# Kernel optimization log

Hardware: AMD Instinct MI355X
Metric: run time of the kernel (lower is better)

Reference implementation:

```python
import jax, jax.numpy as jnp
import numpy as np
from jax import lax

N_NODES = 100000
N_EDGES = 200000
N_GRAPHS = 64
F_IN = 5
HID = 768
EMB = 512
N_LAYERS = 16


def setup_inputs() -> dict:
    key = jax.random.key(0)
    ks = jax.random.split(key, 12)
    s = 0.02
    x = jax.random.normal(ks[0], (N_NODES, F_IN), dtype=jnp.float32)
    edge_index = jax.random.randint(ks[1], (2, N_EDGES), 0, N_NODES, dtype=jnp.int32)
    batch = jnp.sort(jax.random.randint(ks[2], (N_NODES,), 0, N_GRAPHS, dtype=jnp.int32))
    Wp = jax.random.normal(ks[3], (F_IN, HID), dtype=jnp.float32) * s
    bp = jnp.zeros((HID,), dtype=jnp.float32)
    W1 = jax.random.normal(ks[4], (N_LAYERS, HID, HID), dtype=jnp.float32) * s
    b1 = jnp.zeros((N_LAYERS, HID), dtype=jnp.float32)
    W2 = jax.random.normal(ks[5], (N_LAYERS, HID, HID), dtype=jnp.float32) * s
    b2 = jnp.zeros((N_LAYERS, HID), dtype=jnp.float32)
    Wf = jax.random.normal(ks[6], (HID, EMB), dtype=jnp.float32) * s
    bf = jnp.zeros((EMB,), dtype=jnp.float32)
    return {"x": x, "edge_index": edge_index, "batch": batch,
            "Wp": Wp, "bp": bp, "W1": W1, "b1": b1, "W2": W2, "b2": b2,
            "Wf": Wf, "bf": bf}


def reference(x, edge_index, batch, Wp, bp, W1, b1, W2, b2, Wf, bf):
    # input projection: [N, F_IN] -> [N, HID]
    h = x @ Wp + bp
    src, dst = edge_index[0], edge_index[1]

    def layer(h, params):
        w1, bb1, w2, bb2 = params
        # GINConv (eps=0): (1+eps)*x_i + sum_{j->i} x_j, messages flow src -> dst
        agg = jax.ops.segment_sum(h[src], dst, num_segments=N_NODES) + h
        z = jax.nn.relu(agg @ w1 + bb1)
        z = jax.nn.relu(z @ w2 + bb2)
        # outer relu in forward (no-op after ReLU MLP, kept for fidelity)
        return jax.nn.relu(z), None

    h, _ = lax.scan(layer, h, (W1, b1, W2, b2))

    # global mean pool over graphs
    sums = jax.ops.segment_sum(h, batch, num_segments=N_GRAPHS)
    counts = jax.ops.segment_sum(jnp.ones((h.shape[0],), dtype=h.dtype), batch, num_segments=N_GRAPHS)
    pooled = sums / jnp.maximum(counts, 1.0)[:, None]

    return pooled @ Wf + bf
```

## Files before the change

kernel.cpp:

```cpp
#include <hip/hip_runtime.h>

#define HID 768
#define EMB 512
#define NG  64
#define FIN 5
#define NL  16
#define CB  384
#define PSEG 16
#define WPSEG 16

typedef _Float16 f16;
typedef f16   f16x4 __attribute__((ext_vector_type(4)));
typedef f16   f16x8 __attribute__((ext_vector_type(8)));
typedef float f32x4 __attribute__((ext_vector_type(4)));

__global__ void count_deg_k(const int* __restrict__ ei, int* __restrict__ deg, int E) {
    int e = blockIdx.x * 256 + threadIdx.x;
    if (e < E) atomicAdd(&deg[ei[E + e]], 1);
}

__global__ void goff_k(const int* __restrict__ batch, int* __restrict__ goff, int n) {
    int g = threadIdx.x;
    if (g > NG) return;
    if (g == NG) { goff[NG] = n; return; }
    int lo = 0, hi = n;
    while (lo < hi) { int mid = (lo + hi) >> 1; if (batch[mid] < g) lo = mid + 1; else hi = mid; }
    goff[g] = lo;
}

__global__ void scan_rowptr_k(const int* __restrict__ deg, int* __restrict__ rp,
                              int* __restrict__ cur, int n) {
    __shared__ int wsum[16];
    __shared__ int carry;
    int t = threadIdx.x, lane = t & 63, w = t >> 6;
    if (t == 0) carry = 0;
    __syncthreads();
    for (int base = 0; base < n; base += 4096) {
        int v[4]; int s = 0;
        #pragma unroll
        for (int q = 0; q < 4; ++q) { int i = base + t * 4 + q; v[q] = (i < n) ? deg[i] : 0; s += v[q]; }
        int tot = s;
        int sc = tot;
        #pragma unroll
        for (int off = 1; off < 64; off <<= 1) { int u = __shfl_up(sc, off); if (lane >= off) sc += u; }
        if (lane == 63) wsum[w] = sc;
        __syncthreads();
        if (t < 16) {
            int xw = wsum[t];
            #pragma unroll
            for (int off = 1; off < 16; off <<= 1) { int u = __shfl_up(xw, off); if (t >= off) xw += u; }
            wsum[t] = xw;
        }
        __syncthreads();
        int woff = (w > 0) ? wsum[w - 1] : 0;
        int excl = carry + woff + sc - tot;
        #pragma unroll
        for (int q = 0; q < 4; ++q) { int i = base + t * 4 + q; if (i < n) { rp[i] = excl; cur[i] = excl; } excl += v[q]; }
        __syncthreads();
        if (t == 0) carry += wsum[15];
        __syncthreads();
    }
    if (t == 0) rp[n] = carry;
}

__global__ void scatter_k(const int* __restrict__ ei, int* __restrict__ cur,
                          int* __restrict__ csr, int E) {
    int e = blockIdx.x * 256 + threadIdx.x;
    if (e < E) { int d = ei[E + e]; int pos = atomicAdd(&cur[d], 1); csr[pos] = ei[e]; }
}

__global__ void sort_csr_k(const int* __restrict__ rp, int* __restrict__ csr, int n) {
    int i = blockIdx.x * 256 + threadIdx.x;
    if (i >= n) return;
    int e0 = rp[i], e1 = rp[i + 1];
    for (int a = e0 + 1; a < e1; ++a) {
        int v = csr[a];
        int b = a - 1;
        while (b >= e0 && csr[b] > v) { csr[b + 1] = csr[b]; --b; }
        csr[b + 1] = v;
    }
}

__global__ void convert_layer_k(const float* __restrict__ Wa, const float* __restrict__ Wb,
                                f16* __restrict__ wt) {
    __shared__ float tile[64][65];
    const float* src = blockIdx.z ? Wb : Wa;
    f16* dst = wt + (size_t)blockIdx.z * HID * HID;
    int k0 = blockIdx.x * 64, n0 = blockIdx.y * 64;
    int t = threadIdx.x;
    #pragma unroll 4
    for (int i = 0; i < 16; ++i) {
        int r = (t >> 6) + i * 4;
        tile[r][t & 63] = src[(size_t)(k0 + r) * HID + n0 + (t & 63)];
    }
    __syncthreads();
    #pragma unroll 4
    for (int i = 0; i < 16; ++i) {
        int r = (t >> 6) + i * 4;
        dst[(size_t)(n0 + r) * HID + k0 + (t & 63)] = (f16)(tile[t & 63][r] * 64.0f);
    }
}

__global__ void make_wp1_part_k(const float* __restrict__ Wp, const float* __restrict__ bp,
                                const float* __restrict__ W1_0, float* __restrict__ part) {
    int nn = blockIdx.x * 256 + threadIdx.x;
    int s = blockIdx.y;
    if (nn >= HID) return;
    float acc[6] = {0, 0, 0, 0, 0, 0};
    int j0 = s * (HID / WPSEG), j1 = j0 + (HID / WPSEG);
    for (int j = j0; j < j1; ++j) {
        float wj = W1_0[(size_t)j * HID + nn];
        #pragma unroll
        for (int k = 0; k < FIN; ++k) acc[k] += Wp[k * HID + j] * wj;
        acc[5] += bp[j] * wj;
    }
    #pragma unroll
    for (int k = 0; k < 6; ++k) part[((size_t)s * 6 + k) * HID + nn] = acc[k];
}

__global__ void make_wp1_red_k(const float* __restrict__ part, float* __restrict__ wp1) {
    int nn = blockIdx.x * 256 + threadIdx.x;
    if (nn >= HID) return;
    #pragma unroll
    for (int k = 0; k < 6; ++k) {
        float a = 0.0f;
        #pragma unroll
        for (int s = 0; s < WPSEG; ++s) a += part[((size_t)s * 6 + k) * HID + nn];
        wp1[k * HID + nn] = a;
    }
}

__device__ __forceinline__ void row_scale(float amax, float& sc, float& rs) {
    int ex = 10;
    if (amax > 0.0f) frexpf(amax, &ex);
    int sh = 10 - ex;
    sh = sh > 120 ? 120 : (sh < -120 ? -120 : sh);
    sc = ldexpf(1.0f, sh);
    rs = ldexpf(1.0f, -sh);
}

__global__ __launch_bounds__(256) void fused_l0_k(
    const float* __restrict__ x, const int* __restrict__ rp, const int* __restrict__ csr,
    const float* __restrict__ wp1, const float* __restrict__ b1_0,
    f16* __restrict__ h00, f16* __restrict__ h01,
    f16* __restrict__ h10, f16* __restrict__ h11,
    float* __restrict__ rs_out, int nreal, int half) {
    __shared__ float w[7 * HID];
    for (int idx = threadIdx.x; idx < 7 * HID; idx += 256)
        w[idx] = (idx < 6 * HID) ? wp1[idx] : b1_0[idx - 6 * HID];
    __syncthreads();
    int node = blockIdx.x * 4 + (threadIdx.x >> 6);
    int lane = threadIdx.x & 63;
    int cblk = lane >> 5, ll = lane & 31;
    f16* base;
    int rloc;
    if (node < half) { base = cblk ? h10 : h00; rloc = node; }
    else             { base = cblk ? h11 : h01; rloc = node - half; }
    f16* orow = base + (size_t)rloc * CB + ll * 12;
    if (node >= nreal) {
        #pragma unroll
        for (int t = 0; t < 12; ++t) orow[t] = (f16)0.0f;
        if (lane == 0) rs_out[node] = 1.0f;
        return;
    }
    int e0 = rp[node], e1 = rp[node + 1];
    float xa[FIN];
    #pragma unroll
    for (int k = 0; k < FIN; ++k) xa[k] = x[(size_t)node * FIN + k];
    for (int e = e0; e < e1; ++e) {
        int j = csr[e];
        #pragma unroll
        for (int k = 0; k < FIN; ++k) xa[k] += x[(size_t)j * FIN + k];
    }
    float dp1 = (float)(e1 - e0 + 1);
    float a[12];
    #pragma unroll
    for (int t = 0; t < 12; ++t) {
        int c = lane * 12 + t;
        float v = w[5 * HID + c] * dp1 + w[6 * HID + c];
        #pragma unroll
        for (int k = 0; k < FIN; ++k) v += xa[k] * w[k * HID + c];
        a[t] = fmaxf(v, 0.0f);
    }
    float amax = 0.0f;
    #pragma unroll
    for (int t = 0; t < 12; ++t) amax = fmaxf(amax, fabsf(a[t]));
    #pragma unroll
    for (int off = 32; off; off >>= 1) amax = fmaxf(amax, __shfl_xor(amax, off));
    float sc, rs;
    row_scale(amax, sc, rs);
    if (lane == 0) rs_out[node] = rs;
    #pragma unroll
    for (int t = 0; t < 12; ++t) orow[t] = (f16)(a[t] * sc);
}

__global__ __launch_bounds__(256) void aggcol_k(
    const f16* __restrict__ s0, const f16* __restrict__ s1,
    f16* __restrict__ d0, f16* __restrict__ d1,
    const float* __restrict__ rsIn, float inShift,
    float* __restrict__ rsOut, const float* __restrict__ amaxR,
    const int* __restrict__ rp, const int* __restrict__ csr, int nreal, int half,
    int computeScale) {
    int node = blockIdx.x * 8 + (threadIdx.x >> 5);
    int l = threadIdx.x & 31;
    f16* orow = (node < half ? d0 + (size_t)node * CB : d1 + (size_t)(node - half) * CB) + l * 12;
    if (node >= nreal) {
        #pragma unroll
        for (int t = 0; t < 12; ++t) orow[t] = (f16)0.0f;
        if (computeScale && l == 0) rsOut[node] = 1.0f;
        return;
    }
    int e0 = rp[node], e1 = rp[node + 1];
    float invOut;
    if (computeScale) {
        float M = amaxR[node];
        for (int e = e0; e < e1; ++e) M = fmaxf(M, amaxR[csr[e]]);
        float r = 1.0f;
        if (M > 0.0f) {
            int ex; frexpf(M, &ex);
            int sh = ex - 9;
            sh = sh > 120 ? 120 : (sh < -120 ? -120 : sh);
            r = ldexpf(1.0f, sh);
        }
        if (l == 0) rsOut[node] = r;
        invOut = 1.0f / r;
    } else {
        invOut = 1.0f / rsOut[node];
    }
    float a[12];
    {
        float f = rsIn[node] * inShift * invOut;
        const f16* srow = (node < half ? s0 + (size_t)node * CB : s1 + (size_t)(node - half) * CB);
        const f16x4* p = (const f16x4*)(srow + l * 12);
        f16x4 v0 = p[0], v1 = p[1], v2 = p[2];
        #pragma unroll
        for (int t = 0; t < 4; ++t) {
            a[t] = (float)v0[t] * f; a[4 + t] = (float)v1[t] * f; a[8 + t] = (float)v2[t] * f;
        }
    }
    for (int e = e0; e < e1; ++e) {
        int j = csr[e];
        float f = rsIn[j] * inShift * invOut;
        const f16* srow = (j < half ? s0 + (size_t)j * CB : s1 + (size_t)(j - half) * CB);
        const f16x4* p = (const f16x4*)(srow + l * 12);
        f16x4 v0 = p[0], v1 = p[1], v2 = p[2];
        #pragma unroll
        for (int t = 0; t < 4; ++t) {
            a[t] += (float)v0[t] * f; a[4 + t] += (float)v1[t] * f; a[8 + t] += (float)v2[t] * f;
        }
    }
    f16x4 o0, o1, o2;
    #pragma unroll
    for (int t = 0; t < 4; ++t) {
        o0[t] = (f16)a[t]; o1[t] = (f16)a[4 + t]; o2[t] = (f16)a[8 + t];
    }
    f16x4* op = (f16x4*)orow;
    op[0] = o0; op[1] = o1; op[2] = o2;
}

__global__ __launch_bounds__(256) void gemm_seg_k(
    const f16* __restrict__ a0, const f16* __restrict__ a1,
    f16* __restrict__ c0, f16* __restrict__ c1,
    const float* __restrict__ rs, int rsOff, float shiftIn,
    const f16* __restrict__ wt, const float* __restrict__ bias,
    float* __restrict__ amaxR, int recAmax) {
    __shared__ f16 lds[40960];
    const int tid = threadIdx.x;
    const int lane = tid & 63;
    const int wid = tid >> 6;

    const int nwg = gridDim.x;
    const int q = nwg >> 3, r = nwg & 7;
    const int xcd = blockIdx.x & 7, loc = blockIdx.x >> 3;
    const int id2 = (xcd < r ? xcd * (q + 1) : r * (q + 1) + (xcd - r) * q) + loc;
    const int m0 = (id2 / 6) * 128;
    const int n0 = (id2 % 6) * 128;

    const int wr = (wid >> 1) * 64;
    const int wc = (wid & 1) * 64;
    const int lrow = lane >> 3;
    const int usrc = (lane & 7) ^ lrow;
    const int l15 = lane & 15, l4 = lane >> 4;

    auto stageA = [&](int kt, int buf) {
        const f16* abase = (kt < 6) ? a0 : a1;
        const int kb = (kt < 6 ? kt : kt - 6) * 64;
        f16* As = lds + buf * 8192;
        #pragma unroll
        for (int i = 0; i < 4; ++i) {
            int chunk = i * 4 + wid;
            int row = chunk * 8 + lrow;
            const f16* ga = abase + (size_t)(m0 + row) * CB + kb + usrc * 8;
            __builtin_amdgcn_global_load_lds(
                (const __attribute__((address_space(1))) void*)ga,
                (__attribute__((address_space(3))) void*)(As + chunk * 512), 16, 0, 0);
        }
    };
    auto stageB = [&](int kt, int buf) {
        const int kw = kt * 64;
        f16* Bs = lds + 24576 + buf * 8192;
        #pragma unroll
        for (int i = 0; i < 4; ++i) {
            int chunk = i * 4 + wid;
            int row = chunk * 8 + lrow;
            const f16* gb = wt + (size_t)(n0 + row) * HID + kw + usrc * 8;
            __builtin_amdgcn_global_load_lds(
                (const __attribute__((address_space(1))) void*)gb,
                (__attribute__((address_space(3))) void*)(Bs + chunk * 512), 16, 0, 0);
        }
    };

    f32x4 acc[4][4];
    #pragma unroll
    for (int m = 0; m < 4; ++m)
        #pragma unroll
        for (int n = 0; n < 4; ++n) acc[m][n] = (f32x4){0.f, 0.f, 0.f, 0.f};

    stageA(0, 0);
    stageB(0, 0);
    stageA(1, 1);

    #pragma unroll
    for (int t = 0; t < 12; ++t) {
        const f16* Ac = lds + (t % 3) * 8192;
        const f16* Bc = lds + 24576 + (t & 1) * 8192;
        if (t < 11) asm volatile("s_waitcnt vmcnt(4)" ::: "memory");
        else        asm volatile("s_waitcnt vmcnt(0)" ::: "memory");
        __builtin_amdgcn_s_barrier();
        __builtin_amdgcn_sched_barrier(0);
        if (t < 11) stageB(t + 1, (t + 1) & 1);
        if (t < 10) stageA(t + 2, (t + 2) % 3);
        f16x8 af[4][2], bfr[4][2];
        #pragma unroll
        for (int m = 0; m < 4; ++m) {
            int rowH = wr + m * 16 + l15;
            int sw = rowH & 7;
            #pragma unroll
            for (int kk = 0; kk < 2; ++kk) {
                int u = kk * 4 + l4;
                af[m][kk] = *(const f16x8*)(Ac + rowH * 64 + ((u ^ sw) << 3));
            }
        }
        #pragma unroll
        for (int n = 0; n < 4; ++n) {
            int rowB = wc + n * 16 + l15;
            int sw = rowB & 7;
            #pragma unroll
            for (int kk = 0; kk < 2; ++kk) {
                int u = kk * 4 + l4;
                bfr[n][kk] = *(const f16x8*)(Bc + rowB * 64 + ((u ^ sw) << 3));
            }
        }
        __builtin_amdgcn_s_setprio(1);
        #pragma unroll
        for (int kk = 0; kk < 2; ++kk)
            #pragma unroll
            for (int m = 0; m < 4; ++m)
                #pragma unroll
                for (int n = 0; n < 4; ++n)
                    acc[m][n] = __builtin_amdgcn_mfma_f32_16x16x32_f16(af[m][kk], bfr[n][kk], acc[m][n], 0, 0, 0);
        __builtin_amdgcn_s_setprio(0);
    }
    __syncthreads();

    float rvv[16], rinvv[16];
    #pragma unroll
    for (int m = 0; m < 4; ++m)
        #pragma unroll
        for (int r2 = 0; r2 < 4; ++r2) {
            int rowB = wr + m * 16 + (l4 << 2) + r2;
            float rv = rs[rsOff + m0 + rowB] * shiftIn * 8.0f;
            rvv[m * 4 + r2] = rv;
            rinvv[m * 4 + r2] = 1.0f / rv;
        }
    f16* cst = lds;
    float am[16];
    #pragma unroll
    for (int i = 0; i < 16; ++i) am[i] = 0.0f;
    #pragma unroll
    for (int n = 0; n < 4; ++n) {
        const int colB = wc + n * 16 + l15;
        const float bcol = bias[n0 + colB];
        #pragma unroll
        for (int m = 0; m < 4; ++m) {
            #pragma unroll
            for (int r2 = 0; r2 < 4; ++r2) {
                const int rowB = wr + m * 16 + (l4 << 2) + r2;
                float v = acc[m][n][r2] * (1.0f / 512.0f) + bcol * rinvv[m * 4 + r2];
                v = fmaxf(v, 0.0f);
                am[m * 4 + r2] = fmaxf(am[m * 4 + r2], v);
                cst[rowB * 136 + colB] = (f16)v;
            }
        }
    }
    __syncthreads();
    {
        f16* Cw; int csub;
        if (n0 < CB) { Cw = c0; csub = n0; } else { Cw = c1; csub = n0 - CB; }
        #pragma unroll
        for (int i = 0; i < 8; ++i) {
            int rowB = wid * 32 + i * 4 + l4;
            f16x8 vv = *(const f16x8*)&cst[rowB * 136 + l15 * 8];
            *(f16x8*)&Cw[(size_t)(m0 + rowB) * CB + csub + l15 * 8] = vv;
        }
    }
    if (recAmax) {
        #pragma unroll
        for (int i = 0; i < 16; ++i) {
            float a = am[i];
            a = fmaxf(a, __shfl_xor(a, 1));
            a = fmaxf(a, __shfl_xor(a, 2));
            a = fmaxf(a, __shfl_xor(a, 4));
            a = fmaxf(a, __shfl_xor(a, 8));
            if (l15 == 0) {
                int rowB = wr + (i >> 2) * 16 + (l4 << 2) + (i & 3);
                atomicMax((unsigned int*)&amaxR[rsOff + m0 + rowB],
                          __float_as_uint(a * rvv[i]));
            }
        }
    }
}

__global__ __launch_bounds__(256) void pool1_k(
    const f16* __restrict__ h00, const f16* __restrict__ h01,
    const f16* __restrict__ h10, const f16* __restrict__ h11,
    const float* __restrict__ rs,
    const int* __restrict__ goff, float* __restrict__ partial, int half) {
    int g = blockIdx.x, c = blockIdx.y, s = blockIdx.z;
    int t = threadIdx.x;
    int col = c * 256 + t;
    int cb = col >= CB;
    int cc = cb ? col - CB : col;
    int i0 = goff[g], i1 = goff[g + 1];
    int len = i1 - i0;
    int s0 = i0 + (int)(((long long)len * s) / PSEG);
    int s1 = i0 + (int)(((long long)len * (s + 1)) / PSEG);
    float a = 0.0f;
    for (int i = s0; i < s1; ++i) {
        const f16* base = (i < half) ? (cb ? h10 : h00) : (cb ? h11 : h01);
        int r = (i < half) ? i : i - half;
        a += (float)base[(size_t)r * CB + cc] * rs[i];
    }
    partial[((size_t)(g * PSEG + s)) * HID + col] = a;
}

__global__ __launch_bounds__(256) void pool2_k(const float* __restrict__ partial,
                                               float shift, float* __restrict__ pooled) {
    int g = blockIdx.x;
    int col = blockIdx.y * 256 + threadIdx.x;
    float a = 0.0f;
    #pragma unroll
    for (int s = 0; s < PSEG; ++s)
        a += partial[((size_t)(g * PSEG + s)) * HID + col];
    pooled[g * HID + col] = a * shift;
}

__global__ __launch_bounds__(512) void final_mm_k(const float* __restrict__ pooled,
                                                  const int* __restrict__ goff,
                                                  const float* __restrict__ Wf,
                                                  const float* __restrict__ bf,
                                                  float* __restrict__ out) {
    __shared__ float ps[HID];
    int g = blockIdx.x;
    int t = threadIdx.x;
    float inv = 1.0f / fmaxf((float)(goff[g + 1] - goff[g]), 1.0f);
    for (int k = t; k < HID; k += 512) ps[k] = pooled[g * HID + k] * inv;
    __syncthreads();
    float acc = bf[t];
    for (int k = 0; k < HID; ++k) acc += ps[k] * Wf[(size_t)k * EMB + t];
    out[(size_t)g * EMB + t] = acc;
}

__global__ void sentinel_k(float* __restrict__ out, int n, float v) {
    int i = blockIdx.x * 256 + threadIdx.x;
    if (i < n) out[i] = v;
}

extern "C" void kernel_launch(void* const* d_in, const int* in_sizes, int n_in,
                              void* d_out, int out_size, void* d_ws, size_t ws_size,
                              hipStream_t stream) {
    const float* x    = (const float*)d_in[0];
    const int*   ei   = (const int*)d_in[1];
    const int*   batch= (const int*)d_in[2];
    const float* Wp   = (const float*)d_in[3];
    const float* bp   = (const float*)d_in[4];
    const float* W1   = (const float*)d_in[5];
    const float* b1   = (const float*)d_in[6];
    const float* W2   = (const float*)d_in[7];
    const float* b2   = (const float*)d_in[8];
    const float* Wf   = (const float*)d_in[9];
    const float* bf   = (const float*)d_in[10];
    float* out = (float*)d_out;

    const int nreal = in_sizes[0] / FIN;
    const int E     = in_sizes[1] / 2;
    const int npad  = ((nreal + 511) / 512) * 512;
    const int half  = npad / 2;
    const size_t slotsz = (size_t)half * CB;

    char* p = (char*)d_ws;
    auto alloc = [&](size_t bytes) -> char* {
        char* r = p; p += (bytes + 511) & ~(size_t)511; return r;
    };
    f16* slot[6];
    for (int i = 0; i < 6; ++i) slot[i] = (f16*)alloc(slotsz * sizeof(f16));
    f16*   wt   = (f16*)  alloc((size_t)2 * HID * HID * sizeof(f16));
    float* rsA  = (float*)alloc((size_t)npad * sizeof(float));
    float* rsB  = (float*)alloc((size_t)npad * sizeof(float));
    float* amaxR= (float*)alloc((size_t)npad * sizeof(float));
    int*   rp   = (int*)  alloc((size_t)(npad + 1) * sizeof(int));
    int*   csr  = (int*)  alloc((size_t)E * sizeof(int));
    float* wp1  = (float*)alloc((size_t)6 * HID * sizeof(float));
    float* wp1p = (float*)alloc((size_t)WPSEG * 6 * HID * sizeof(float));
    int*   goff = (int*)  alloc((size_t)(NG + 1) * sizeof(int));
    float* pooled = (float*)alloc((size_t)NG * HID * sizeof(float));
    float* partial = (float*)alloc((size_t)NG * PSEG * HID * sizeof(float));
    char*  zstart = p;
    int*   deg  = (int*)  alloc((size_t)npad * sizeof(int));
    int*   cur  = (int*)  alloc((size_t)npad * sizeof(int));
    size_t zbytes = (size_t)(p - zstart);
    size_t need  = (size_t)(p - (char*)d_ws);

    if (need > ws_size) {
        sentinel_k<<<(out_size + 255) / 256, 256, 0, stream>>>(out, out_size, (float)(ws_size >> 20));
        return;
    }

    hipMemsetAsync(zstart, 0, zbytes, stream);

    count_deg_k  <<<(E + 255) / 256, 256, 0, stream>>>(ei, deg, E);
    goff_k       <<<1, 128, 0, stream>>>(batch, goff, nreal);
    scan_rowptr_k<<<1, 1024, 0, stream>>>(deg, rp, cur, nreal);
    scatter_k    <<<(E + 255) / 256, 256, 0, stream>>>(ei, cur, csr, E);
    sort_csr_k   <<<(nreal + 255) / 256, 256, 0, stream>>>(rp, csr, nreal);

    make_wp1_part_k<<<dim3(3, WPSEG), 256, 0, stream>>>(Wp, bp, W1, wp1p);
    make_wp1_red_k <<<3, 256, 0, stream>>>(wp1p, wp1);

    f16 *h00 = slot[0], *h01 = slot[1], *h10 = slot[2], *h11 = slot[3];
    f16 *f0 = slot[4], *f1 = slot[5];

    fused_l0_k<<<npad / 4, 256, 0, stream>>>(x, rp, csr, wp1, b1, h00, h01, h10, h11, rsA, nreal, half);

    const int nwg = (half / 128) * (HID / 128);

    convert_layer_k<<<dim3(HID / 64, HID / 64, 2), 256, 0, stream>>>(W1, W2, wt);
    hipMemsetAsync(amaxR, 0, (size_t)npad * sizeof(float), stream);
    gemm_seg_k<<<nwg, 256, 0, stream>>>(h00, h10, f0, f1, rsA, 0, 1.0f,
                                        wt + (size_t)HID * HID, b2, amaxR, 1);
    gemm_seg_k<<<nwg, 256, 0, stream>>>(h01, h11, h00, h10, rsA, half, 1.0f,
                                        wt + (size_t)HID * HID, b2, amaxR, 1);
    { f16 *n00 = f0, *n10 = f1, *n01 = h00, *n11 = h10, *nf0 = h01, *nf1 = h11;
      h00 = n00; h10 = n10; h01 = n01; h11 = n11; f0 = nf0; f1 = nf1; }

    float* rcur = rsA;
    float  shift = 8.0f;

    for (int l = 1; l < NL; ++l) {
        convert_layer_k<<<dim3(HID / 64, HID / 64, 2), 256, 0, stream>>>(
            W1 + (size_t)l * HID * HID, W2 + (size_t)l * HID * HID, wt);
        float* rnew = (rcur == rsA) ? rsB : rsA;
        aggcol_k<<<npad / 8, 256, 0, stream>>>(h00, h01, f0, f1, rcur, shift, rnew, amaxR,
                                               rp, csr, nreal, half, 1);
        aggcol_k<<<npad / 8, 256, 0, stream>>>(h10, h11, h00, h01, rcur, shift, rnew, amaxR,
                                               rp, csr, nreal, half, 0);
        f16 *g00 = f0, *g01 = f1, *g10 = h00, *g11 = h01, *x0 = h10, *x1 = h11;
        gemm_seg_k<<<nwg, 256, 0, stream>>>(g00, g10, x0, x1, rnew, 0, 1.0f,
                                            wt, b1 + (size_t)l * HID, amaxR, 0);
        gemm_seg_k<<<nwg, 256, 0, stream>>>(g01, g11, g00, g10, rnew, half, 1.0f,
                                            wt, b1 + (size_t)l * HID, amaxR, 0);
        f16 *z00 = x0, *z10 = x1, *z01 = g00, *z11 = g10;
        hipMemsetAsync(amaxR, 0, (size_t)npad * sizeof(float), stream);
        gemm_seg_k<<<nwg, 256, 0, stream>>>(z00, z10, g01, g11, rnew, 0, 8.0f,
                                            wt + (size_t)HID * HID, b2 + (size_t)l * HID, amaxR, 1);
        gemm_seg_k<<<nwg, 256, 0, stream>>>(z01, z11, z00, z10, rnew, half, 8.0f,
                                            wt + (size_t)HID * HID, b2 + (size_t)l * HID, amaxR, 1);
        h00 = g01; h10 = g11; h01 = z00; h11 = z10; f0 = g00; f1 = g10;
        rcur = rnew;
        shift = 64.0f;
    }

    pool1_k<<<dim3(NG, HID / 256, PSEG), 256, 0, stream>>>(h00, h01, h10, h11, rcur, goff, partial, half);
    pool2_k<<<dim3(NG, HID / 256), 256, 0, stream>>>(partial, shift, pooled);
    final_mm_k<<<NG, 512, 0, stream>>>(pooled, goff, Wf, bf, out);
}
```

Before: 6.565 ms.

## Load GEMM B fragments directly from global into registers, shrink LDS

```diff
diff --git a/kernel.cpp b/kernel.cpp
--- a/kernel.cpp
+++ b/kernel.cpp
@@ -258,13 +258,13 @@
     op[0] = o0; op[1] = o1; op[2] = o2;
 }
 
-__global__ __launch_bounds__(256) void gemm_seg_k(
+__global__ __launch_bounds__(256, 3) void gemm_seg_k(
     const f16* __restrict__ a0, const f16* __restrict__ a1,
     f16* __restrict__ c0, f16* __restrict__ c1,
     const float* __restrict__ rs, int rsOff, float shiftIn,
     const f16* __restrict__ wt, const float* __restrict__ bias,
     float* __restrict__ amaxR, int recAmax) {
-    __shared__ f16 lds[40960];
+    __shared__ f16 lds[17408];
     const int tid = threadIdx.x;
     const int lane = tid & 63;
     const int wid = tid >> 6;
@@ -296,18 +296,15 @@
                 (__attribute__((address_space(3))) void*)(As + chunk * 512), 16, 0, 0);
         }
     };
-    auto stageB = [&](int kt, int buf) {
-        const int kw = kt * 64;
-        f16* Bs = lds + 24576 + buf * 8192;
-        #pragma unroll
-        for (int i = 0; i < 4; ++i) {
-            int chunk = i * 4 + wid;
-            int row = chunk * 8 + lrow;
-            const f16* gb = wt + (size_t)(n0 + row) * HID + kw + usrc * 8;
-            __builtin_amdgcn_global_load_lds(
-                (const __attribute__((address_space(1))) void*)gb,
-                (__attribute__((address_space(3))) void*)(Bs + chunk * 512), 16, 0, 0);
-        }
+
+    f16x8 bfr[4][2];
+    auto loadB = [&](int kt) {
+        #pragma unroll
+        for (int n = 0; n < 4; ++n)
+            #pragma unroll
+            for (int kk = 0; kk < 2; ++kk)
+                bfr[n][kk] = *(const f16x8*)(wt + (size_t)(n0 + wc + n * 16 + l15) * HID
+                                             + kt * 64 + (kk * 4 + l4) * 8);
     };
 
     f32x4 acc[4][4];
@@ -317,20 +314,16 @@
         for (int n = 0; n < 4; ++n) acc[m][n] = (f32x4){0.f, 0.f, 0.f, 0.f};
 
     stageA(0, 0);
-    stageB(0, 0);
-    stageA(1, 1);
+    loadB(0);
 
     #pragma unroll
     for (int t = 0; t < 12; ++t) {
-        const f16* Ac = lds + (t % 3) * 8192;
-        const f16* Bc = lds + 24576 + (t & 1) * 8192;
-        if (t < 11) asm volatile("s_waitcnt vmcnt(4)" ::: "memory");
-        else        asm volatile("s_waitcnt vmcnt(0)" ::: "memory");
+        asm volatile("s_waitcnt vmcnt(8)" ::: "memory");
         __builtin_amdgcn_s_barrier();
         __builtin_amdgcn_sched_barrier(0);
-        if (t < 11) stageB(t + 1, (t + 1) & 1);
-        if (t < 10) stageA(t + 2, (t + 2) % 3);
-        f16x8 af[4][2], bfr[4][2];
+        if (t < 11) stageA(t + 1, (t + 1) & 1);
+        const f16* Ac = lds + (t & 1) * 8192;
+        f16x8 af[4][2];
         #pragma unroll
         for (int m = 0; m < 4; ++m) {
             int rowH = wr + m * 16 + l15;
@@ -341,16 +334,6 @@
                 af[m][kk] = *(const f16x8*)(Ac + rowH * 64 + ((u ^ sw) << 3));
             }
         }
-        #pragma unroll
-        for (int n = 0; n < 4; ++n) {
-            int rowB = wc + n * 16 + l15;
-            int sw = rowB & 7;
-            #pragma unroll
-            for (int kk = 0; kk < 2; ++kk) {
-                int u = kk * 4 + l4;
-                bfr[n][kk] = *(const f16x8*)(Bc + rowB * 64 + ((u ^ sw) << 3));
-            }
-        }
         __builtin_amdgcn_s_setprio(1);
         #pragma unroll
         for (int kk = 0; kk < 2; ++kk)
@@ -360,6 +343,7 @@
                 for (int n = 0; n < 4; ++n)
                     acc[m][n] = __builtin_amdgcn_mfma_f32_16x16x32_f16(af[m][kk], bfr[n][kk], acc[m][n], 0, 0, 0);
         __builtin_amdgcn_s_setprio(0);
+        if (t < 11) loadB(t + 1);
     }
     __syncthreads();
 
```

Result: slower. 10.13 ms (+54.2%).
